# Optimization experiments

Measured on AMD Instinct MI355X. Metric: run time of the kernel, lower is better.

## Reference

```python
import jax, jax.numpy as jnp
import numpy as np

N_NODES = 100000
N_FEATS = 256
OUT_DIM = 64
NNZ_X = 1280000
N_EDGES = 1600000
KEEP_PROB = 0.9  # 1 - dropout_rate (dropout_rate = 0.1)


def setup_inputs() -> dict:
    key = jax.random.key(0)
    ks = jax.random.split(key, 7)
    feat_values = jax.random.normal(ks[0], (NNZ_X,), dtype=jnp.float32)
    feat_rows = jax.random.randint(ks[1], (NNZ_X,), 0, N_NODES, dtype=jnp.int32)
    feat_cols = jax.random.randint(ks[2], (NNZ_X,), 0, N_FEATS, dtype=jnp.int32)
    # GlorotNormal kernel: std = sqrt(2 / (fan_in + fan_out))
    glorot_std = float(np.sqrt(2.0 / (N_FEATS + OUT_DIM)))
    kernel = jax.random.normal(ks[3], (N_FEATS, OUT_DIM), dtype=jnp.float32) * glorot_std
    adj_values = jax.random.uniform(ks[4], (N_EDGES,), dtype=jnp.float32)
    adj_rows = jax.random.randint(ks[5], (N_EDGES,), 0, N_NODES, dtype=jnp.int32)
    adj_cols = jax.random.randint(ks[6], (N_EDGES,), 0, N_NODES, dtype=jnp.int32)
    return {
        "feat_values": feat_values,
        "kernel": kernel,
        "adj_values": adj_values,
        "feat_rows": feat_rows,
        "feat_cols": feat_cols,
        "adj_rows": adj_rows,
        "adj_cols": adj_cols,
    }


def reference(feat_values, kernel, adj_values, feat_rows, feat_cols, adj_rows, adj_cols):
    # sparse dropout on feature values (training=True path), deterministic key.
    # tf: keep = floor(keep_prob + U[0,1)) cast to bool; retain then scale 1/keep_prob
    u = jax.random.uniform(jax.random.key(42), feat_values.shape, dtype=feat_values.dtype)
    keep = jnp.floor(KEEP_PROB + u).astype(bool)
    v = jnp.where(keep, feat_values, jnp.zeros_like(feat_values)) * (1.0 / KEEP_PROB)

    # SpMM 1: XW[n, o] = sum_{(n,f) in X} v * kernel[f, o]
    xw = jax.ops.segment_sum(v[:, None] * kernel[feat_cols], feat_rows,
                             num_segments=N_NODES)  # [N, OUT]

    # SpMM 2: out[i, o] = sum_{(i,j) in A} a_ij * xw[j, o]
    agg = jax.ops.segment_sum(adj_values[:, None] * xw[adj_cols], adj_rows,
                              num_segments=N_NODES)  # [N, OUT]

    return jax.nn.relu(agg)
```

## Files before the change

### kernel.cpp

```cpp
#include <hip/hip_runtime.h>

#define N_NODES 100000
#define N_FEATS 256
#define OUT_DIM 64
#define NNZ_X   1280000
#define N_EDGES 1600000
#define NBH     782
#define CHUNK   4096
#define KPT     8
#define CAPXH   2560
#define CAPAH   3072

__device__ __forceinline__ unsigned rotl32(unsigned x, unsigned d) {
    return (x << d) | (x >> (32u - d));
}

__device__ __forceinline__ float jax_uniform_42(unsigned e) {
    unsigned x0 = 0u, x1 = e;
    const unsigned ks0 = 0u, ks1 = 42u, ks2 = 0u ^ 42u ^ 0x1BD11BDAu;
    x0 += ks0; x1 += ks1;
#define TF_R(r) { x0 += x1; x1 = rotl32(x1, r); x1 ^= x0; }
    TF_R(13) TF_R(15) TF_R(26) TF_R(6)
    x0 += ks1; x1 += ks2 + 1u;
    TF_R(17) TF_R(29) TF_R(16) TF_R(24)
    x0 += ks2; x1 += ks0 + 2u;
    TF_R(13) TF_R(15) TF_R(26) TF_R(6)
    x0 += ks0; x1 += ks1 + 3u;
    TF_R(17) TF_R(29) TF_R(16) TF_R(24)
    x0 += ks1; x1 += ks2 + 4u;
    TF_R(13) TF_R(15) TF_R(26) TF_R(6)
    x0 += ks2; x1 += ks0 + 5u;
#undef TF_R
    unsigned bits = x0 ^ x1;
    return __uint_as_float((bits >> 9) | 0x3f800000u) - 1.0f;
}

__device__ __forceinline__ bool keep_42(unsigned e) {
    float u = jax_uniform_42(e);
    return floorf(0.9f + u) != 0.0f;
}

__device__ __forceinline__ unsigned short f32_bf16(float f) {
    unsigned bits = __float_as_uint(f);
    return (unsigned short)((bits + 0x7fffu + ((bits >> 16) & 1u)) >> 16);
}

__device__ __forceinline__ float bflo(unsigned u) { return __uint_as_float(u << 16); }
__device__ __forceinline__ float bfhi(unsigned u) { return __uint_as_float(u & 0xffff0000u); }

__global__ __launch_bounds__(512) void phase1(
        const float* __restrict__ fvals, const int* __restrict__ frows,
        const int* __restrict__ fcols,
        const float* __restrict__ avals, const int* __restrict__ arows,
        const int* __restrict__ acols,
        int* __restrict__ bcur_x, int* __restrict__ bcur_a,
        float2* __restrict__ gx, float2* __restrict__ ga) {
    const int isA = blockIdx.y;
    const float* vals = isA ? avals : fvals;
    const int* rows   = isA ? arows : frows;
    const int* cols   = isA ? acols : fcols;
    int* bcur         = isA ? bcur_a : bcur_x;
    float2* dst       = isA ? ga : gx;
    const unsigned cap = isA ? CAPAH : CAPXH;
    const unsigned n  = isA ? N_EDGES : NNZ_X;

    unsigned t = threadIdx.x;
    unsigned base = blockIdx.x * CHUNK;
    if (base >= n) return;

    __shared__ int cnt[1024];
    __shared__ int start[1024];
    __shared__ int gofs[NBH];
    __shared__ int wtot[8];
    __shared__ int s_nvalid;
    __shared__ unsigned long long payload[CHUNK];
    __shared__ unsigned short bkt[CHUNK];

    int   rcache[KPT];
    float vcache[KPT];
    int   ccache[KPT];

    cnt[t] = 0;
    cnt[t + 512] = 0;
    __syncthreads();
    #pragma unroll
    for (int k = 0; k < KPT; k++) {
        unsigned i = base + k * 512u + t;
        int r = -1;
        if (i < n) {
            int rr = rows[i];
            float v = vals[i];
            int   c = cols[i];
            if (isA || keep_42(i)) {
                r = rr;
                vcache[k] = isA ? v : v * (float)(1.0 / 0.9);
                ccache[k] = c;
            }
        }
        rcache[k] = r;
        if (r >= 0) atomicAdd(&cnt[(unsigned)r >> 7], 1);
    }
    __syncthreads();
    unsigned lane = t & 63u, wid = t >> 6;
    int c0 = cnt[2 * t], c1 = cnt[2 * t + 1];
    int pairsum = c0 + c1;
    int inc = pairsum;
    #pragma unroll
    for (int d = 1; d < 64; d <<= 1) {
        int v = __shfl_up(inc, d, 64);
        if (lane >= (unsigned)d) inc += v;
    }
    if (lane == 63u) wtot[wid] = inc;
    __syncthreads();
    int offw = 0;
    #pragma unroll
    for (int w = 0; w < 8; w++) if ((unsigned)w < wid) offw += wtot[w];
    int excl = offw + inc - pairsum;
    start[2 * t]     = excl;
    start[2 * t + 1] = excl + c0;
    if (t == 511u) s_nvalid = excl + pairsum;
    __syncthreads();
    for (unsigned bb = t; bb < NBH; bb += 512u) {
        int cb = cnt[bb];
        if (cb > 0) {
            int g = atomicAdd(&bcur[bb], cb);
            gofs[bb] = g - start[bb];
        }
    }
    __syncthreads();
    int n_valid = s_nvalid;
    #pragma unroll
    for (int k = 0; k < KPT; k++) {
        int r = rcache[k];
        if (r >= 0) {
            unsigned b = (unsigned)r >> 7;
            int p = atomicAdd(&start[b], 1);
            unsigned packed = ((unsigned)ccache[k] << 7) | ((unsigned)r & 127u);
            payload[p] = ((unsigned long long)__float_as_uint(vcache[k]) << 32) | packed;
            bkt[p] = (unsigned short)b;
        }
    }
    __syncthreads();
    #pragma unroll
    for (int k = 0; k < KPT; k++) {
        int sidx = k * 512 + (int)t;
        if (sidx < n_valid) {
            unsigned b = bkt[sidx];
            unsigned long long m = payload[sidx];
            float2 e;
            e.x = __uint_as_float((unsigned)(m >> 32));
            e.y = __int_as_float((int)(unsigned)m);
            dst[(size_t)b * cap + gofs[b] + sidx] = e;
        }
    }
}

__global__ __launch_bounds__(512) void sort_x_spmm1(
        const int* __restrict__ bcur_x, const float2* __restrict__ gx,
        const float* __restrict__ W, unsigned short* __restrict__ xw) {
    __shared__ float2 ent[CAPXH];
    __shared__ int hist[128];
    __shared__ int starts[128];
    __shared__ int cursor[128];
    __shared__ int wtot[2];
    unsigned t = threadIdx.x;
    unsigned wid = t >> 6, lane = t & 63u;
    unsigned b = blockIdx.x;
    int cnt = bcur_x[b];
    const float2* src = gx + (size_t)b * CAPXH;

    if (t < 128) hist[t] = 0;
    __syncthreads();
    float2 ec[5];
    #pragma unroll
    for (int k = 0; k < 5; k++) {
        int i = k * 512 + (int)t;
        if (i < cnt) {
            float2 e = src[i];
            ec[k] = e;
            atomicAdd(&hist[((unsigned)__float_as_int(e.y)) & 127u], 1);
        }
    }
    __syncthreads();
    int inc = 0, binv = 0;
    if (wid < 2u) {
        unsigned bin = wid * 64u + lane;
        binv = hist[bin];
        inc = binv;
        #pragma unroll
        for (int d = 1; d < 64; d <<= 1) {
            int v = __shfl_up(inc, d, 64);
            if (lane >= (unsigned)d) inc += v;
        }
        if (lane == 63u) wtot[wid] = inc;
    }
    __syncthreads();
    if (wid < 2u) {
        unsigned bin = wid * 64u + lane;
        int excl = inc - binv + (wid == 1u ? wtot[0] : 0);
        starts[bin] = excl;
        cursor[bin] = excl;
    }
    __syncthreads();
    #pragma unroll
    for (int k = 0; k < 5; k++) {
        int i = k * 512 + (int)t;
        if (i < cnt) {
            float2 e = ec[k];
            int pos = atomicAdd(&cursor[((unsigned)__float_as_int(e.y)) & 127u], 1);
            ent[pos] = e;
        }
    }
    __syncthreads();
    unsigned quarter = lane >> 4, sub = lane & 15u;
    const float4* W4 = (const float4*)W;
    ushort4* xw4 = (ushort4*)xw;
    for (unsigned r = wid; r < 128u; r += 8u) {
        int s0 = starts[r];
        int s1 = (r == 127u) ? cnt : starts[r + 1];
        float4 acc[4];
        #pragma unroll
        for (int j = 0; j < 4; j++) { acc[j].x = acc[j].y = acc[j].z = acc[j].w = 0.0f; }
        int p = s0;
        for (; p + 16 <= s1; p += 16) {
            float2 e[4];
            #pragma unroll
            for (int j = 0; j < 4; j++) e[j] = ent[p + 4 * quarter + j];
            float4 w[4];
            #pragma unroll
            for (int j = 0; j < 4; j++)
                w[j] = W4[(((unsigned)__float_as_int(e[j].y)) >> 7) * 16u + sub];
            #pragma unroll
            for (int j = 0; j < 4; j++) {
                acc[j].x = fmaf(e[j].x, w[j].x, acc[j].x);
                acc[j].y = fmaf(e[j].x, w[j].y, acc[j].y);
                acc[j].z = fmaf(e[j].x, w[j].z, acc[j].z);
                acc[j].w = fmaf(e[j].x, w[j].w, acc[j].w);
            }
        }
        for (int q = p + (int)quarter; q < s1; q += 4) {
            float2 e = ent[q];
            float4 w = W4[(((unsigned)__float_as_int(e.y)) >> 7) * 16u + sub];
            acc[0].x = fmaf(e.x, w.x, acc[0].x);
            acc[0].y = fmaf(e.x, w.y, acc[0].y);
            acc[0].z = fmaf(e.x, w.z, acc[0].z);
            acc[0].w = fmaf(e.x, w.w, acc[0].w);
        }
        float ax = (acc[0].x + acc[1].x) + (acc[2].x + acc[3].x);
        float ay = (acc[0].y + acc[1].y) + (acc[2].y + acc[3].y);
        float az = (acc[0].z + acc[1].z) + (acc[2].z + acc[3].z);
        float aw = (acc[0].w + acc[1].w) + (acc[2].w + acc[3].w);
        ax += __shfl(ax, (int)(lane ^ 16u), 64);
        ay += __shfl(ay, (int)(lane ^ 16u), 64);
        az += __shfl(az, (int)(lane ^ 16u), 64);
        aw += __shfl(aw, (int)(lane ^ 16u), 64);
        ax += __shfl(ax, (int)(lane ^ 32u), 64);
        ay += __shfl(ay, (int)(lane ^ 32u), 64);
        az += __shfl(az, (int)(lane ^ 32u), 64);
        aw += __shfl(aw, (int)(lane ^ 32u), 64);
        unsigned grow = (b << 7) + r;
        if (quarter == 0 && grow < N_NODES) {
            ushort4 o;
            o.x = f32_bf16(ax); o.y = f32_bf16(ay);
            o.z = f32_bf16(az); o.w = f32_bf16(aw);
            xw4[(size_t)grow * 16u + sub] = o;
        }
    }
}

__global__ __launch_bounds__(512) void sort_a_spmm2(
        const int* __restrict__ bcur_a, const float2* __restrict__ ga,
        const unsigned short* __restrict__ xw, float* __restrict__ out) {
    __shared__ float2 ent[CAPAH];
    __shared__ int hist[128];
    __shared__ int starts[128];
    __shared__ int cursor[128];
    __shared__ int wtot[2];
    unsigned t = threadIdx.x;
    unsigned wid = t >> 6, lane = t & 63u;
    unsigned b = blockIdx.x;
    int cnt = bcur_a[b];
    const float2* src = ga + (size_t)b * CAPAH;

    if (t < 128) hist[t] = 0;
    __syncthreads();
    float2 ec[6];
    #pragma unroll
    for (int k = 0; k < 6; k++) {
        int i = k * 512 + (int)t;
        if (i < cnt) {
            float2 e = src[i];
            ec[k] = e;
            atomicAdd(&hist[((unsigned)__float_as_int(e.y)) & 127u], 1);
        }
    }
    __syncthreads();
    int inc = 0, binv = 0;
    if (wid < 2u) {
        unsigned bin = wid * 64u + lane;
        binv = hist[bin];
        inc = binv;
        #pragma unroll
        for (int d = 1; d < 64; d <<= 1) {
            int v = __shfl_up(inc, d, 64);
            if (lane >= (unsigned)d) inc += v;
        }
        if (lane == 63u) wtot[wid] = inc;
    }
    __syncthreads();
    if (wid < 2u) {
        unsigned bin = wid * 64u + lane;
        int excl = inc - binv + (wid == 1u ? wtot[0] : 0);
        starts[bin] = excl;
        cursor[bin] = excl;
    }
    __syncthreads();
    #pragma unroll
    for (int k = 0; k < 6; k++) {
        int i = k * 512 + (int)t;
        if (i < cnt) {
            float2 e = ec[k];
            int pos = atomicAdd(&cursor[((unsigned)__float_as_int(e.y)) & 127u], 1);
            ent[pos] = e;
        }
    }
    __syncthreads();
    unsigned oct = lane >> 3, sub = lane & 7u;
    const uint4* xw8 = (const uint4*)xw;
    for (unsigned r = wid; r < 128u; r += 8u) {
        int s0 = starts[r];
        int s1 = (r == 127u) ? cnt : starts[r + 1];
        float acc[8];
        #pragma unroll
        for (int j = 0; j < 8; j++) acc[j] = 0.0f;
        int p = s0 + (int)oct;
        for (; p + 8 < s1; p += 16) {
            float2 e0 = ent[p];
            float2 e1 = ent[p + 8];
            uint4 u0 = xw8[(((unsigned)__float_as_int(e0.y)) >> 7) * 8u + sub];
            uint4 u1 = xw8[(((unsigned)__float_as_int(e1.y)) >> 7) * 8u + sub];
            float v0 = e0.x, v1 = e1.x;
            acc[0] = fmaf(v0, bflo(u0.x), acc[0]);
            acc[1] = fmaf(v0, bfhi(u0.x), acc[1]);
            acc[2] = fmaf(v0, bflo(u0.y), acc[2]);
            acc[3] = fmaf(v0, bfhi(u0.y), acc[3]);
            acc[4] = fmaf(v0, bflo(u0.z), acc[4]);
            acc[5] = fmaf(v0, bfhi(u0.z), acc[5]);
            acc[6] = fmaf(v0, bflo(u0.w), acc[6]);
            acc[7] = fmaf(v0, bfhi(u0.w), acc[7]);
            acc[0] = fmaf(v1, bflo(u1.x), acc[0]);
            acc[1] = fmaf(v1, bfhi(u1.x), acc[1]);
            acc[2] = fmaf(v1, bflo(u1.y), acc[2]);
            acc[3] = fmaf(v1, bfhi(u1.y), acc[3]);
            acc[4] = fmaf(v1, bflo(u1.z), acc[4]);
            acc[5] = fmaf(v1, bfhi(u1.z), acc[5]);
            acc[6] = fmaf(v1, bflo(u1.w), acc[6]);
            acc[7] = fmaf(v1, bfhi(u1.w), acc[7]);
        }
        if (p < s1) {
            float2 e = ent[p];
            uint4 u = xw8[(((unsigned)__float_as_int(e.y)) >> 7) * 8u + sub];
            float v = e.x;
            acc[0] = fmaf(v, bflo(u.x), acc[0]);
            acc[1] = fmaf(v, bfhi(u.x), acc[1]);
            acc[2] = fmaf(v, bflo(u.y), acc[2]);
            acc[3] = fmaf(v, bfhi(u.y), acc[3]);
            acc[4] = fmaf(v, bflo(u.z), acc[4]);
            acc[5] = fmaf(v, bfhi(u.z), acc[5]);
            acc[6] = fmaf(v, bflo(u.w), acc[6]);
            acc[7] = fmaf(v, bfhi(u.w), acc[7]);
        }
        #pragma unroll
        for (int j = 0; j < 8; j++) {
            acc[j] += __shfl_xor(acc[j], 8, 64);
            acc[j] += __shfl_xor(acc[j], 16, 64);
            acc[j] += __shfl_xor(acc[j], 32, 64);
        }
        unsigned grow = (b << 7) + r;
        if (oct == 0 && grow < N_NODES) {
            float4 o0, o1;
            o0.x = fmaxf(acc[0], 0.0f);
            o0.y = fmaxf(acc[1], 0.0f);
            o0.z = fmaxf(acc[2], 0.0f);
            o0.w = fmaxf(acc[3], 0.0f);
            o1.x = fmaxf(acc[4], 0.0f);
            o1.y = fmaxf(acc[5], 0.0f);
            o1.z = fmaxf(acc[6], 0.0f);
            o1.w = fmaxf(acc[7], 0.0f);
            float4* op = (float4*)(out + (size_t)grow * 64u + sub * 8u);
            op[0] = o0;
            op[1] = o1;
        }
    }
}

extern "C" void kernel_launch(void* const* d_in, const int* in_sizes, int n_in,
                              void* d_out, int out_size, void* d_ws, size_t ws_size,
                              hipStream_t stream) {
    const float* feat_values = (const float*)d_in[0];
    const float* W           = (const float*)d_in[1];
    const float* adj_values  = (const float*)d_in[2];
    const int*   feat_rows   = (const int*)d_in[3];
    const int*   feat_cols   = (const int*)d_in[4];
    const int*   adj_rows    = (const int*)d_in[5];
    const int*   adj_cols    = (const int*)d_in[6];
    float* out = (float*)d_out;

    char* ws = (char*)d_ws;
    int* bcur_x = (int*)(ws + 0);
    int* bcur_a = (int*)(ws + 4096);
    float2* gx  = (float2*)(ws + 16384);
    float2* ga  = (float2*)(ws + 16384 + 16015360);
    unsigned short* xw = (unsigned short*)(ws + 35250176);

    hipMemsetAsync(ws, 0, 8192, stream);

    dim3 gp1((N_EDGES + CHUNK - 1) / CHUNK, 2);
    phase1<<<gp1, 512, 0, stream>>>(feat_values, feat_rows, feat_cols,
                                    adj_values, adj_rows, adj_cols,
                                    bcur_x, bcur_a, gx, ga);
    sort_x_spmm1<<<NBH, 512, 0, stream>>>(bcur_x, gx, W, xw);
    sort_a_spmm2<<<NBH, 512, 0, stream>>>(bcur_a, ga, xw, out);
}
```

Baseline: 181.2 us.

## Store XW in four column slices and gather per slice in SpMM2

The first SpMM now writes the bf16 XW matrix as four column slices of 16 outputs each, so each row slice takes 32 bytes, with a padded row count. The second SpMM loops over the four slices and runs its full edge gather for one slice at a time. Each lane loads one packed pair per edge and writes a float2 of ReLU output. The goal is to shrink the gathered working set per pass (about 3.2 MB per slice) so random neighbour reads hit in L2 more often. The cost is four passes over the sorted LDS edge list, narrower 4-byte loads, and more loop and shuffle overhead.

```diff
diff --git a/kernel.cpp b/kernel.cpp
--- a/kernel.cpp
+++ b/kernel.cpp
@@ -10,6 +10,7 @@
 #define KPT     8
 #define CAPXH   2560
 #define CAPAH   3072
+#define XW_ROWS 100096
 
 __device__ __forceinline__ unsigned rotl32(unsigned x, unsigned d) {
     return (x << d) | (x >> (32u - d));
@@ -214,7 +215,7 @@
     __syncthreads();
     unsigned quarter = lane >> 4, sub = lane & 15u;
     const float4* W4 = (const float4*)W;
-    ushort4* xw4 = (ushort4*)xw;
+    uint2* xws = (uint2*)xw;
     for (unsigned r = wid; r < 128u; r += 8u) {
         int s0 = starts[r];
         int s1 = (r == 127u) ? cnt : starts[r + 1];
@@ -260,10 +261,11 @@
         aw += __shfl(aw, (int)(lane ^ 32u), 64);
         unsigned grow = (b << 7) + r;
         if (quarter == 0 && grow < N_NODES) {
-            ushort4 o;
-            o.x = f32_bf16(ax); o.y = f32_bf16(ay);
-            o.z = f32_bf16(az); o.w = f32_bf16(aw);
-            xw4[(size_t)grow * 16u + sub] = o;
+            unsigned sl = sub >> 2;
+            uint2 q2;
+            q2.x = (unsigned)f32_bf16(ax) | ((unsigned)f32_bf16(ay) << 16);
+            q2.y = (unsigned)f32_bf16(az) | ((unsigned)f32_bf16(aw) << 16);
+            xws[(size_t)sl * (XW_ROWS * 4u) + grow * 4u + (sub & 3u)] = q2;
         }
     }
 }
@@ -326,70 +328,44 @@
     }
     __syncthreads();
     unsigned oct = lane >> 3, sub = lane & 7u;
-    const uint4* xw8 = (const uint4*)xw;
-    for (unsigned r = wid; r < 128u; r += 8u) {
-        int s0 = starts[r];
-        int s1 = (r == 127u) ? cnt : starts[r + 1];
-        float acc[8];
-        #pragma unroll
-        for (int j = 0; j < 8; j++) acc[j] = 0.0f;
-        int p = s0 + (int)oct;
-        for (; p + 8 < s1; p += 16) {
-            float2 e0 = ent[p];
-            float2 e1 = ent[p + 8];
-            uint4 u0 = xw8[(((unsigned)__float_as_int(e0.y)) >> 7) * 8u + sub];
-            uint4 u1 = xw8[(((unsigned)__float_as_int(e1.y)) >> 7) * 8u + sub];
-            float v0 = e0.x, v1 = e1.x;
-            acc[0] = fmaf(v0, bflo(u0.x), acc[0]);
-            acc[1] = fmaf(v0, bfhi(u0.x), acc[1]);
-            acc[2] = fmaf(v0, bflo(u0.y), acc[2]);
-            acc[3] = fmaf(v0, bfhi(u0.y), acc[3]);
-            acc[4] = fmaf(v0, bflo(u0.z), acc[4]);
-            acc[5] = fmaf(v0, bfhi(u0.z), acc[5]);
-            acc[6] = fmaf(v0, bflo(u0.w), acc[6]);
-            acc[7] = fmaf(v0, bfhi(u0.w), acc[7]);
-            acc[0] = fmaf(v1, bflo(u1.x), acc[0]);
-            acc[1] = fmaf(v1, bfhi(u1.x), acc[1]);
-            acc[2] = fmaf(v1, bflo(u1.y), acc[2]);
-            acc[3] = fmaf(v1, bfhi(u1.y), acc[3]);
-            acc[4] = fmaf(v1, bflo(u1.z), acc[4]);
-            acc[5] = fmaf(v1, bfhi(u1.z), acc[5]);
-            acc[6] = fmaf(v1, bflo(u1.w), acc[6]);
-            acc[7] = fmaf(v1, bfhi(u1.w), acc[7]);
-        }
-        if (p < s1) {
-            float2 e = ent[p];
-            uint4 u = xw8[(((unsigned)__float_as_int(e.y)) >> 7) * 8u + sub];
-            float v = e.x;
-            acc[0] = fmaf(v, bflo(u.x), acc[0]);
-            acc[1] = fmaf(v, bfhi(u.x), acc[1]);
-            acc[2] = fmaf(v, bflo(u.y), acc[2]);
-            acc[3] = fmaf(v, bfhi(u.y), acc[3]);
-            acc[4] = fmaf(v, bflo(u.z), acc[4]);
-            acc[5] = fmaf(v, bfhi(u.z), acc[5]);
-            acc[6] = fmaf(v, bflo(u.w), acc[6]);
-            acc[7] = fmaf(v, bfhi(u.w), acc[7]);
-        }
-        #pragma unroll
-        for (int j = 0; j < 8; j++) {
-            acc[j] += __shfl_xor(acc[j], 8, 64);
-            acc[j] += __shfl_xor(acc[j], 16, 64);
-            acc[j] += __shfl_xor(acc[j], 32, 64);
-        }
-        unsigned grow = (b << 7) + r;
-        if (oct == 0 && grow < N_NODES) {
-            float4 o0, o1;
-            o0.x = fmaxf(acc[0], 0.0f);
-            o0.y = fmaxf(acc[1], 0.0f);
-            o0.z = fmaxf(acc[2], 0.0f);
-            o0.w = fmaxf(acc[3], 0.0f);
-            o1.x = fmaxf(acc[4], 0.0f);
-            o1.y = fmaxf(acc[5], 0.0f);
-            o1.z = fmaxf(acc[6], 0.0f);
-            o1.w = fmaxf(acc[7], 0.0f);
-            float4* op = (float4*)(out + (size_t)grow * 64u + sub * 8u);
-            op[0] = o0;
-            op[1] = o1;
+    #pragma unroll 1
+    for (unsigned sl = 0; sl < 4u; sl++) {
+        const unsigned* xwp = (const unsigned*)xw + (size_t)sl * (XW_ROWS * 8u);
+        #pragma unroll 1
+        for (unsigned r = wid; r < 128u; r += 8u) {
+            int s0 = starts[r];
+            int s1 = (r == 127u) ? cnt : starts[r + 1];
+            float a0 = 0.0f, a1 = 0.0f;
+            int p = s0 + (int)oct;
+            for (; p + 8 < s1; p += 16) {
+                float2 e0 = ent[p];
+                float2 e1 = ent[p + 8];
+                unsigned u0 = xwp[(((unsigned)__float_as_int(e0.y)) >> 7) * 8u + sub];
+                unsigned u1 = xwp[(((unsigned)__float_as_int(e1.y)) >> 7) * 8u + sub];
+                a0 = fmaf(e0.x, bflo(u0), a0);
+                a1 = fmaf(e0.x, bfhi(u0), a1);
+                a0 = fmaf(e1.x, bflo(u1), a0);
+                a1 = fmaf(e1.x, bfhi(u1), a1);
+            }
+            if (p < s1) {
+                float2 e = ent[p];
+                unsigned u = xwp[(((unsigned)__float_as_int(e.y)) >> 7) * 8u + sub];
+                a0 = fmaf(e.x, bflo(u), a0);
+                a1 = fmaf(e.x, bfhi(u), a1);
+            }
+            a0 += __shfl_xor(a0, 8, 64);
+            a1 += __shfl_xor(a1, 8, 64);
+            a0 += __shfl_xor(a0, 16, 64);
+            a1 += __shfl_xor(a1, 16, 64);
+            a0 += __shfl_xor(a0, 32, 64);
+            a1 += __shfl_xor(a1, 32, 64);
+            unsigned grow = (b << 7) + r;
+            if (oct == 0 && grow < N_NODES) {
+                float2 o;
+                o.x = fmaxf(a0, 0.0f);
+                o.y = fmaxf(a1, 0.0f);
+                *(float2*)(out + (size_t)grow * 64u + sl * 16u + sub * 2u) = o;
+            }
         }
     }
 }
```

Result: slower. 205.5 us (+13.5%).
